# Performance work log

Measured on AMD Instinct MI355X. Metric: run time of the kernel, lower is better.

## Reference

```python
import jax, jax.numpy as jnp
import numpy as np

DIM = 768
NUM_HEADS = 12
DECAY_RATE = 5.0


def setup_inputs() -> dict:
    key = jax.random.key(0)
    k1, k2, k3, k4 = jax.random.split(key, 4)
    B, N, C = 4, 1024, DIM
    x = jax.random.normal(k1, (B, N, C), dtype=jnp.float32)
    # torch nn.Linear weights: y = x @ W.T ; qkv_bias=False
    qkv_w = jax.random.normal(k2, (3 * C, C), dtype=jnp.float32) * (1.0 / np.sqrt(C))
    proj_w = jax.random.normal(k3, (C, C), dtype=jnp.float32) * (1.0 / np.sqrt(C))
    proj_b = jax.random.normal(k4, (C,), dtype=jnp.float32) * 0.01
    return {"x": x, "qkv_w": qkv_w, "proj_w": proj_w, "proj_b": proj_b, "cur_epoch": 3}


def reference(x, qkv_w, proj_w, proj_b, cur_epoch):
    B, N, C = x.shape
    H = NUM_HEADS
    hd = C // H
    scale = hd ** -0.5

    qkv = (x @ qkv_w.T).reshape(B, N, 3, H, hd).transpose(2, 0, 3, 1, 4)  # [3,B,H,N,hd]
    q, k, v = qkv[0], qkv[1], qkv[2]

    scores = jnp.einsum("bhqd,bhkd->bhqk", q, k) * scale
    logp = jax.nn.log_softmax(scores, axis=-1)
    attn = jnp.exp(logp)  # [B,H,N,N]

    # Per-key entropy: column j of attn flattened over (B,H,N) is renormalized
    # by Categorical; dividing by num_heads cancels under normalization.
    # H(p/s) = log(s) - (1/s) * sum(p * log p)
    s = jnp.sum(attn, axis=(0, 1, 2))                 # [N]
    plogp = jnp.sum(attn * logp, axis=(0, 1, 2))      # [N]
    entropies = jnp.log(s) - plogp / s

    # threshold decay: factor = sum_{i=0}^{cur_epoch-1} decay*exp(-(i+1))
    factor = DECAY_RATE * float(np.sum(np.exp(-(np.arange(cur_epoch) + 1.0))))
    entropy_threshold = float(np.log(C)) - factor

    # attn[:,:,:,keep] @ v[:,:,keep,:] == (attn * mask) @ v  (zeroed columns drop out)
    mask = (entropies <= entropy_threshold).astype(attn.dtype)  # [N]
    out = jnp.einsum("bhqk,bhkd->bhqd", attn * mask[None, None, None, :], v)
    out = out.transpose(0, 2, 1, 3).reshape(B, N, C)
    out = out @ proj_w.T + proj_b
    return out
```

## Files before the change

kernel.cpp:

```cpp
#include <hip/hip_runtime.h>


typedef __bf16 bf16x8 __attribute__((ext_vector_type(8)));
typedef __bf16 bf16x4 __attribute__((ext_vector_type(4)));
typedef float  f32x4  __attribute__((ext_vector_type(4)));

#define MFMA16(a, b, c) __builtin_amdgcn_mfma_f32_16x16x32_bf16((a), (b), (c), 0, 0, 0)
#define LOG2E_8 0.18033688f

__device__ __forceinline__ void ld_glds16(const __bf16* g, __bf16* s) {
  __builtin_amdgcn_global_load_lds(
      (const __attribute__((address_space(1))) unsigned int*)g,
      (__attribute__((address_space(3))) unsigned int*)s, 16, 0, 0);
}

__global__ __launch_bounds__(256) void kc_conv(
    const float* __restrict__ x, const float* __restrict__ qw, const float* __restrict__ pw,
    __bf16* __restrict__ xb, __bf16* __restrict__ qwb, __bf16* __restrict__ pwb,
    float* __restrict__ colSP, int* __restrict__ keepCnt)
{
  const int i = blockIdx.x * 256 + threadIdx.x;
  const float4* src;
  __bf16* dst;
  int j;
  if (i < 786432)       { src = (const float4*)x;  dst = xb;  j = i; }
  else if (i < 1228800) { src = (const float4*)qw; dst = qwb; j = i - 786432; }
  else                  { src = (const float4*)pw; dst = pwb; j = i - 1228800; }
  const float4 f = src[j];
  bf16x4 o;
  o[0] = (__bf16)f.x; o[1] = (__bf16)f.y; o[2] = (__bf16)f.z; o[3] = (__bf16)f.w;
  *(bf16x4*)(dst + 4 * (size_t)j) = o;
  if (i < 2048) colSP[i] = 0.f;
  if (i == 0) *keepCnt = 0;
}

__global__ __launch_bounds__(256) void kg_qkv(
    const __bf16* __restrict__ A, const __bf16* __restrict__ Bm,
    __bf16* __restrict__ qb, __bf16* __restrict__ kb, float* __restrict__ v)
{
  __shared__ __bf16 As[128 * 64];
  __shared__ __bf16 Bs[128 * 64];
  const int tid = threadIdx.x;
  const int w = tid >> 6, lane = tid & 63, quad = lane >> 4, l = lane & 15;
  const int wm = w >> 1, wn = w & 1;
  const int r0 = blockIdx.y * 128, c0 = blockIdx.x * 128;
  const int srow = lane >> 3, skk = (lane & 7) * 8;

  f32x4 acc[4][4] = {};

  for (int k0 = 0; k0 < 768; k0 += 64) {
    if (k0) __syncthreads();
#pragma unroll
    for (int s = 0; s < 4; ++s) {
      const int si = w * 4 + s;
      const int row = si * 8 + srow;
      ld_glds16(A + (size_t)(r0 + row) * 768 + k0 + skk, &As[si * 512]);
      ld_glds16(Bm + (size_t)(c0 + row) * 768 + k0 + skk, &Bs[si * 512]);
    }
    __syncthreads();
#pragma unroll
    for (int kk = 0; kk < 2; ++kk) {
      bf16x8 af[4], bf[4];
#pragma unroll
      for (int t = 0; t < 4; ++t) {
        af[t] = *(const bf16x8*)&As[(wm * 64 + t * 16 + l) * 64 + kk * 32 + quad * 8];
        bf[t] = *(const bf16x8*)&Bs[(wn * 64 + t * 16 + l) * 64 + kk * 32 + quad * 8];
      }
#pragma unroll
      for (int mt = 0; mt < 4; ++mt)
#pragma unroll
        for (int nt = 0; nt < 4; ++nt)
          acc[mt][nt] = MFMA16(af[mt], bf[nt], acc[mt][nt]);
    }
  }

  const int part = c0 / 768;
  const int cbase = c0 % 768;
#pragma unroll
  for (int mt = 0; mt < 4; ++mt) {
#pragma unroll
    for (int nt = 0; nt < 4; ++nt) {
      const int cc = cbase + wn * 64 + nt * 16 + l;
      const int h = cc >> 6, d = cc & 63;
#pragma unroll
      for (int i = 0; i < 4; ++i) {
        const int rg = r0 + wm * 64 + mt * 16 + quad * 4 + i;
        const int b_ = rg >> 10, n = rg & 1023;
        const size_t off = ((size_t)(b_ * 12 + h) * 1024 + n) * 64 + d;
        const float val = acc[mt][nt][i];
        if (part == 0)      qb[off] = (__bf16)val;
        else if (part == 1) kb[off] = (__bf16)val;
        else                v[off]  = val;
      }
    }
  }
}

__global__ __launch_bounds__(256) void ks_fused(
    const __bf16* __restrict__ qb, const __bf16* __restrict__ kb,
    float* __restrict__ lse, float* __restrict__ colSP)
{
  __shared__ __bf16 Ks[2][64 * 72];
  __shared__ float sS[1024];
  __shared__ float sP[1024];
  __shared__ float zrow[64];
  const int tid = threadIdx.x;
  const int w = tid >> 6, lane = tid & 63, quad = lane >> 4, l = lane & 15;
  const int bh = blockIdx.x, r0 = blockIdx.y * 64;
  const int row = tid >> 3, ko = (tid & 7) * 8;
  for (int i = tid; i < 1024; i += 256) { sS[i] = 0.f; sP[i] = 0.f; }
  if (tid < 64) zrow[tid] = 0.f;

  const __bf16* qbase = qb + ((size_t)bh * 1024 + r0 + l) * 64;
  bf16x8 aq0[4], aq1[4];
#pragma unroll
  for (int rt = 0; rt < 4; ++rt) {
    aq0[rt] = *(const bf16x8*)(qbase + rt * 1024 + quad * 8);
    aq1[rt] = *(const bf16x8*)(qbase + rt * 1024 + 32 + quad * 8);
  }
  const __bf16* kbase = kb + (size_t)bh * 65536;
  const f32x4 zero = {0.f, 0.f, 0.f, 0.f};
  const int koff = (w * 16 + l) * 72 + quad * 8;

  uint4 ka0 = *(const uint4*)(kbase + (size_t)row * 64 + ko);
  uint4 ka1 = *(const uint4*)(kbase + (size_t)(row + 32) * 64 + ko);

  float z[16] = {};
  for (int s = 0; s < 16; ++s) {
    __bf16* Kw = Ks[s & 1];
    *(uint4*)&Kw[row * 72 + ko] = ka0;
    *(uint4*)&Kw[(row + 32) * 72 + ko] = ka1;
    __syncthreads();
    const int nxt = (s + 1) & 15;
    ka0 = *(const uint4*)(kbase + (size_t)(nxt * 64 + row) * 64 + ko);
    ka1 = *(const uint4*)(kbase + (size_t)(nxt * 64 + row + 32) * 64 + ko);
    const bf16x8 kf0 = *(const bf16x8*)&Kw[koff];
    const bf16x8 kf1 = *(const bf16x8*)&Kw[koff + 32];
#pragma unroll
    for (int rt = 0; rt < 4; ++rt) {
      f32x4 acc = MFMA16(aq0[rt], kf0, zero);
      acc = MFMA16(aq1[rt], kf1, acc);
#pragma unroll
      for (int r = 0; r < 4; ++r) z[rt * 4 + r] += exp2f(acc[r] * LOG2E_8);
    }
  }
#pragma unroll
  for (int off = 1; off < 16; off <<= 1) {
#pragma unroll
    for (int i = 0; i < 16; ++i) z[i] += __shfl_xor(z[i], off);
  }
  if (l == 0) {
#pragma unroll
    for (int rt = 0; rt < 4; ++rt)
#pragma unroll
      for (int r = 0; r < 4; ++r)
        atomicAdd(&zrow[rt * 16 + quad * 4 + r], z[rt * 4 + r]);
  }
  __syncthreads();
  if (tid < 64) lse[bh * 1024 + r0 + tid] = __logf(zrow[tid]);
  float nlb[16], nlg[16];
#pragma unroll
  for (int rt = 0; rt < 4; ++rt) {
#pragma unroll
    for (int r = 0; r < 4; ++r) {
      const float Z = zrow[rt * 16 + quad * 4 + r];
      const float lg = __logf(Z);
      nlg[rt * 4 + r] = -lg;
      nlb[rt * 4 + r] = -lg * 1.44269504f;
    }
  }

  for (int s = 0; s < 16; ++s) {
    __bf16* Kw = Ks[s & 1];
    *(uint4*)&Kw[row * 72 + ko] = ka0;
    *(uint4*)&Kw[(row + 32) * 72 + ko] = ka1;
    __syncthreads();
    if (s < 15) {
      ka0 = *(const uint4*)(kbase + (size_t)((s + 1) * 64 + row) * 64 + ko);
      ka1 = *(const uint4*)(kbase + (size_t)((s + 1) * 64 + row + 32) * 64 + ko);
    }
    const bf16x8 kf0 = *(const bf16x8*)&Kw[koff];
    const bf16x8 kf1 = *(const bf16x8*)&Kw[koff + 32];
    float cs = 0.f, cp = 0.f;
#pragma unroll
    for (int rt = 0; rt < 4; ++rt) {
      f32x4 acc = MFMA16(aq0[rt], kf0, zero);
      acc = MFMA16(aq1[rt], kf1, acc);
#pragma unroll
      for (int r = 0; r < 4; ++r) {
        const float a = acc[r];
        const float t = exp2f(fmaf(a, LOG2E_8, nlb[rt * 4 + r]));
        const float d = fmaf(a, 0.125f, nlg[rt * 4 + r]);
        cs += t;
        cp = fmaf(t, d, cp);
      }
    }
    cs += __shfl_xor(cs, 16); cs += __shfl_xor(cs, 32);
    cp += __shfl_xor(cp, 16); cp += __shfl_xor(cp, 32);
    if (lane < 16) {
      sS[s * 64 + w * 16 + l] += cs;
      sP[s * 64 + w * 16 + l] += cp;
    }
  }
  __syncthreads();
  for (int i = tid; i < 1024; i += 256) {
    atomicAdd(&colSP[i], sS[i]);
    atomicAdd(&colSP[1024 + i], sP[i]);
  }
}

__global__ void k_mask(const float* __restrict__ colSP, const int* __restrict__ cur_epoch,
                       float* __restrict__ mask, int* __restrict__ keepCnt)
{
  const int j = threadIdx.x;
  const float s = colSP[j];
  const float ent = __logf(s) - colSP[1024 + j] / s;
  const int ce = cur_epoch[0];
  float factor = 0.f;
  for (int i = 1; i <= ce; ++i) factor += __expf(-(float)i);
  factor *= 5.0f;
  const float thr = __logf(768.0f) - factor;
  const int keep = (ent <= thr) ? 1 : 0;
  mask[j] = keep ? 1.0f : 0.0f;
  if (keep) atomicAdd(keepCnt, 1);
}

__global__ __launch_bounds__(256) void k_av(
    const __bf16* __restrict__ qb, const __bf16* __restrict__ kb,
    const float* __restrict__ v, const float* __restrict__ lse,
    const float* __restrict__ mask, const int* __restrict__ keepCnt,
    __bf16* __restrict__ ctxb)
{
  if (*keepCnt == 0) return;
  const int tid = threadIdx.x;
  const int bh = blockIdx.x, r0 = blockIdx.y * 32;
  const int b_ = bh / 12, h = bh % 12;
  __shared__ float qs[32][64];
  __shared__ float pbuf[4][8][64];
  for (int i = tid; i < 2048; i += 256)
    qs[i >> 6][i & 63] = (float)qb[((size_t)bh * 1024 + r0) * 64 + i];
  __syncthreads();
  const int w = tid >> 6, l = tid & 63, rb = w * 8;
  float ls[8];
#pragma unroll
  for (int i = 0; i < 8; ++i) ls[i] = lse[bh * 1024 + r0 + rb + i];
  float acc[8] = {};
  for (int chunk = 0; chunk < 16; ++chunk) {
    const float mk = mask[chunk * 64 + l];
    if (__ballot(mk != 0.0f) == 0ull) continue;
    const __bf16* kp = kb + ((size_t)bh * 1024 + chunk * 64 + l) * 64;
    float s[8] = {};
    for (int d0 = 0; d0 < 64; d0 += 8) {
      const bf16x8 kf = *(const bf16x8*)(kp + d0);
#pragma unroll
      for (int dd = 0; dd < 8; ++dd) {
        const float kv = (float)kf[dd];
#pragma unroll
        for (int i = 0; i < 8; ++i) s[i] += qs[rb + i][d0 + dd] * kv;
      }
    }
    __syncthreads();
#pragma unroll
    for (int i = 0; i < 8; ++i)
      pbuf[w][i][l] = __expf(s[i] * 0.125f - ls[i]) * mk;
    __syncthreads();
    const float* vp = v + ((size_t)bh * 1024 + chunk * 64) * 64 + l;
    for (int jj = 0; jj < 64; ++jj) {
      const float vv = vp[(size_t)jj * 64];
#pragma unroll
      for (int i = 0; i < 8; ++i) acc[i] += pbuf[w][i][jj] * vv;
    }
  }
#pragma unroll
  for (int i = 0; i < 8; ++i)
    ctxb[((size_t)(b_ * 1024 + r0 + rb + i)) * 768 + h * 64 + l] = (__bf16)acc[i];
}

__global__ __launch_bounds__(256) void kg_proj(
    const __bf16* __restrict__ A, const __bf16* __restrict__ Bm,
    const float* __restrict__ bias, const int* __restrict__ keepCnt,
    float* __restrict__ out)
{
  const int tid = threadIdx.x;
  const int w = tid >> 6, lane = tid & 63, quad = lane >> 4, l = lane & 15;
  const int r0 = blockIdx.y * 64, c0 = blockIdx.x * 64;
  if (*keepCnt == 0) {
#pragma unroll
    for (int ct = 0; ct < 4; ++ct) {
      const int c = c0 + ct * 16 + l;
      const float bv = bias[c];
#pragma unroll
      for (int i = 0; i < 4; ++i) {
        const int rg = r0 + w * 16 + quad * 4 + i;
        out[(size_t)rg * 768 + c] = bv;
      }
    }
    return;
  }
  __shared__ __bf16 As[64 * 72];
  __shared__ __bf16 Bs[64 * 72];
  const int row = tid >> 3, ko = (tid & 7) * 8;
  const f32x4 zero = {0.f, 0.f, 0.f, 0.f};
  f32x4 acc[4];
#pragma unroll
  for (int ct = 0; ct < 4; ++ct) acc[ct] = zero;

  uint4 a0 = *(const uint4*)(A + (size_t)(r0 + row) * 768 + ko);
  uint4 a1 = *(const uint4*)(A + (size_t)(r0 + row + 32) * 768 + ko);
  uint4 b0 = *(const uint4*)(Bm + (size_t)(c0 + row) * 768 + ko);
  uint4 b1 = *(const uint4*)(Bm + (size_t)(c0 + row + 32) * 768 + ko);

  for (int k0 = 0; k0 < 768; k0 += 64) {
    __syncthreads();
    *(uint4*)&As[row * 72 + ko] = a0;
    *(uint4*)&As[(row + 32) * 72 + ko] = a1;
    *(uint4*)&Bs[row * 72 + ko] = b0;
    *(uint4*)&Bs[(row + 32) * 72 + ko] = b1;
    __syncthreads();
    if (k0 < 704) {
      a0 = *(const uint4*)(A + (size_t)(r0 + row) * 768 + k0 + 64 + ko);
      a1 = *(const uint4*)(A + (size_t)(r0 + row + 32) * 768 + k0 + 64 + ko);
      b0 = *(const uint4*)(Bm + (size_t)(c0 + row) * 768 + k0 + 64 + ko);
      b1 = *(const uint4*)(Bm + (size_t)(c0 + row + 32) * 768 + k0 + 64 + ko);
    }
    const bf16x8 af0 = *(const bf16x8*)&As[(w * 16 + l) * 72 + quad * 8];
    const bf16x8 af1 = *(const bf16x8*)&As[(w * 16 + l) * 72 + 32 + quad * 8];
#pragma unroll
    for (int ct = 0; ct < 4; ++ct) {
      const bf16x8 bf0 = *(const bf16x8*)&Bs[(ct * 16 + l) * 72 + quad * 8];
      const bf16x8 bf1 = *(const bf16x8*)&Bs[(ct * 16 + l) * 72 + 32 + quad * 8];
      acc[ct] = MFMA16(af0, bf0, acc[ct]);
      acc[ct] = MFMA16(af1, bf1, acc[ct]);
    }
  }
#pragma unroll
  for (int ct = 0; ct < 4; ++ct) {
    const int c = c0 + ct * 16 + l;
#pragma unroll
    for (int i = 0; i < 4; ++i) {
      const int rg = r0 + w * 16 + quad * 4 + i;
      out[(size_t)rg * 768 + c] = acc[ct][i] + bias[c];
    }
  }
}

extern "C" void kernel_launch(void* const* d_in, const int* in_sizes, int n_in,
                              void* d_out, int out_size, void* d_ws, size_t ws_size,
                              hipStream_t stream)
{
  const float* x      = (const float*)d_in[0];
  const float* qkv_w  = (const float*)d_in[1];
  const float* proj_w = (const float*)d_in[2];
  const float* proj_b = (const float*)d_in[3];
  const int*   cur_ep = (const int*)d_in[4];

  char* W = (char*)d_ws;
  __bf16* xb    = (__bf16*)(W + 0);
  __bf16* qwb   = (__bf16*)(W + 6291456);
  __bf16* pwb   = (__bf16*)(W + 9830400);
  __bf16* qb    = (__bf16*)(W + 11010048);
  __bf16* kb    = (__bf16*)(W + 17301504);
  float*  v     = (float*) (W + 23592960);
  __bf16* ctxb  = (__bf16*)(W + 36175872);
  float*  lse   = (float*) (W + 42467328);
  float*  mask  = (float*) (W + 42663936);
  int*    keep  = (int*)   (W + 42668032);
  float*  colSP = (float*) (W + 42668544);
  float*  out   = (float*)d_out;

  kc_conv<<<5376, 256, 0, stream>>>(x, qkv_w, proj_w, xb, qwb, pwb, colSP, keep);
  kg_qkv<<<dim3(18, 32), 256, 0, stream>>>(xb, qwb, qb, kb, v);
  ks_fused<<<dim3(48, 16), 256, 0, stream>>>(qb, kb, lse, colSP);
  k_mask<<<1, 1024, 0, stream>>>(colSP, cur_ep, mask, keep);
  k_av<<<dim3(48, 32), 256, 0, stream>>>(qb, kb, v, lse, mask, keep, ctxb);
  kg_proj<<<dim3(12, 64), 256, 0, stream>>>(ctxb, pwb, proj_b, keep, out);
}
```

Measured before the change: 161.1 us.

## Load K fragments directly from global and double wave count in score kernel

The score/statistics kernel drops the shared-memory K staging and its per-step barriers. Each wave now loads its own K MFMA fragments straight from global memory with register prefetch. Blocks grow to 512 threads (8 waves), each covering 128 keys per step over 8 steps instead of 16. This removes LDS traffic and __syncthreads in the inner loops, at the cost of uncoalesced 16-byte global loads and higher register pressure per block.

```diff
diff --git a/kernel.cpp b/kernel.cpp
--- a/kernel.cpp
+++ b/kernel.cpp
@@ -96,20 +96,19 @@
   }
 }
 
-__global__ __launch_bounds__(256) void ks_fused(
+__global__ __launch_bounds__(512) void ks_fused(
     const __bf16* __restrict__ qb, const __bf16* __restrict__ kb,
     float* __restrict__ lse, float* __restrict__ colSP)
 {
-  __shared__ __bf16 Ks[2][64 * 72];
   __shared__ float sS[1024];
   __shared__ float sP[1024];
   __shared__ float zrow[64];
   const int tid = threadIdx.x;
   const int w = tid >> 6, lane = tid & 63, quad = lane >> 4, l = lane & 15;
   const int bh = blockIdx.x, r0 = blockIdx.y * 64;
-  const int row = tid >> 3, ko = (tid & 7) * 8;
-  for (int i = tid; i < 1024; i += 256) { sS[i] = 0.f; sP[i] = 0.f; }
+  for (int i = tid; i < 1024; i += 512) { sS[i] = 0.f; sP[i] = 0.f; }
   if (tid < 64) zrow[tid] = 0.f;
+  __syncthreads();
 
   const __bf16* qbase = qb + ((size_t)bh * 1024 + r0 + l) * 64;
   bf16x8 aq0[4], aq1[4];
@@ -118,28 +117,22 @@
     aq0[rt] = *(const bf16x8*)(qbase + rt * 1024 + quad * 8);
     aq1[rt] = *(const bf16x8*)(qbase + rt * 1024 + 32 + quad * 8);
   }
-  const __bf16* kbase = kb + (size_t)bh * 65536;
+  const __bf16* kfrag = kb + (size_t)bh * 65536 + (size_t)(w * 16 + l) * 64 + quad * 8;
   const f32x4 zero = {0.f, 0.f, 0.f, 0.f};
-  const int koff = (w * 16 + l) * 72 + quad * 8;
-
-  uint4 ka0 = *(const uint4*)(kbase + (size_t)row * 64 + ko);
-  uint4 ka1 = *(const uint4*)(kbase + (size_t)(row + 32) * 64 + ko);
+
+  bf16x8 kf0 = *(const bf16x8*)(kfrag);
+  bf16x8 kf1 = *(const bf16x8*)(kfrag + 32);
 
   float z[16] = {};
-  for (int s = 0; s < 16; ++s) {
-    __bf16* Kw = Ks[s & 1];
-    *(uint4*)&Kw[row * 72 + ko] = ka0;
-    *(uint4*)&Kw[(row + 32) * 72 + ko] = ka1;
-    __syncthreads();
-    const int nxt = (s + 1) & 15;
-    ka0 = *(const uint4*)(kbase + (size_t)(nxt * 64 + row) * 64 + ko);
-    ka1 = *(const uint4*)(kbase + (size_t)(nxt * 64 + row + 32) * 64 + ko);
-    const bf16x8 kf0 = *(const bf16x8*)&Kw[koff];
-    const bf16x8 kf1 = *(const bf16x8*)&Kw[koff + 32];
+  for (int s = 0; s < 8; ++s) {
+    const bf16x8 c0 = kf0, c1 = kf1;
+    const int nxt = (s + 1) & 7;
+    kf0 = *(const bf16x8*)(kfrag + (size_t)nxt * 8192);
+    kf1 = *(const bf16x8*)(kfrag + (size_t)nxt * 8192 + 32);
 #pragma unroll
     for (int rt = 0; rt < 4; ++rt) {
-      f32x4 acc = MFMA16(aq0[rt], kf0, zero);
-      acc = MFMA16(aq1[rt], kf1, acc);
+      f32x4 acc = MFMA16(aq0[rt], c0, zero);
+      acc = MFMA16(aq1[rt], c1, acc);
 #pragma unroll
       for (int r = 0; r < 4; ++r) z[rt * 4 + r] += exp2f(acc[r] * LOG2E_8);
     }
@@ -170,22 +163,17 @@
     }
   }
 
-  for (int s = 0; s < 16; ++s) {
-    __bf16* Kw = Ks[s & 1];
-    *(uint4*)&Kw[row * 72 + ko] = ka0;
-    *(uint4*)&Kw[(row + 32) * 72 + ko] = ka1;
-    __syncthreads();
-    if (s < 15) {
-      ka0 = *(const uint4*)(kbase + (size_t)((s + 1) * 64 + row) * 64 + ko);
-      ka1 = *(const uint4*)(kbase + (size_t)((s + 1) * 64 + row + 32) * 64 + ko);
-    }
-    const bf16x8 kf0 = *(const bf16x8*)&Kw[koff];
-    const bf16x8 kf1 = *(const bf16x8*)&Kw[koff + 32];
+  for (int s = 0; s < 8; ++s) {
+    const bf16x8 c0 = kf0, c1 = kf1;
+    if (s < 7) {
+      kf0 = *(const bf16x8*)(kfrag + (size_t)(s + 1) * 8192);
+      kf1 = *(const bf16x8*)(kfrag + (size_t)(s + 1) * 8192 + 32);
+    }
     float cs = 0.f, cp = 0.f;
 #pragma unroll
     for (int rt = 0; rt < 4; ++rt) {
-      f32x4 acc = MFMA16(aq0[rt], kf0, zero);
-      acc = MFMA16(aq1[rt], kf1, acc);
+      f32x4 acc = MFMA16(aq0[rt], c0, zero);
+      acc = MFMA16(aq1[rt], c1, acc);
 #pragma unroll
       for (int r = 0; r < 4; ++r) {
         const float a = acc[r];
@@ -198,12 +186,12 @@
     cs += __shfl_xor(cs, 16); cs += __shfl_xor(cs, 32);
     cp += __shfl_xor(cp, 16); cp += __shfl_xor(cp, 32);
     if (lane < 16) {
-      sS[s * 64 + w * 16 + l] += cs;
-      sP[s * 64 + w * 16 + l] += cp;
+      sS[s * 128 + w * 16 + l] += cs;
+      sP[s * 128 + w * 16 + l] += cp;
     }
   }
   __syncthreads();
-  for (int i = tid; i < 1024; i += 256) {
+  for (int i = tid; i < 1024; i += 512) {
     atomicAdd(&colSP[i], sS[i]);
     atomicAdd(&colSP[1024 + i], sP[i]);
   }
@@ -370,7 +358,7 @@
 
   kc_conv<<<5376, 256, 0, stream>>>(x, qkv_w, proj_w, xb, qwb, pwb, colSP, keep);
   kg_qkv<<<dim3(18, 32), 256, 0, stream>>>(xb, qwb, qb, kb, v);
-  ks_fused<<<dim3(48, 16), 256, 0, stream>>>(qb, kb, lse, colSP);
+  ks_fused<<<dim3(48, 16), 512, 0, stream>>>(qb, kb, lse, colSP);
   k_mask<<<1, 1024, 0, stream>>>(colSP, cur_ep, mask, keep);
   k_av<<<dim3(48, 32), 256, 0, stream>>>(qb, kb, v, lse, mask, keep, ctxb);
   kg_proj<<<dim3(12, 64), 256, 0, stream>>>(ctxb, pwb, proj_b, keep, out);
```

New measurement: 159.2 us. About the same (-1.1%).
